# Optimization experiments

Hardware: AMD Instinct MI355X
Metric: run time of the kernel (lower is better)

The kernel has to match this reference:

```python
import jax, jax.numpy as jnp
import numpy as np

SCALE = 1.0  # module scale=1; dropout_p=0 so dropout is identity; selector is Identity


def setup_inputs() -> dict:
    key = jax.random.key(0)
    k0, k1, k2, k3, k4 = jax.random.split(key, 5)
    B, S, DIN, DOUT, P, R = 4, 2048, 4096, 4096, 5, 8
    x = jax.random.normal(k0, (B, S, DIN), dtype=jnp.float32)
    W = jax.random.normal(k1, (DOUT, DIN), dtype=jnp.float32) * 0.02   # nn.Linear weight [out, in]
    lora_down = jax.random.normal(k2, (P, DIN, R), dtype=jnp.float32) * 0.02
    lora_up = jax.random.normal(k3, (P, R, DOUT), dtype=jnp.float32) * 0.02
    lora_route = jax.random.normal(k4, (P, DIN, P), dtype=jnp.float32) * 0.02
    return {"x": x, "W": W, "lora_down": lora_down, "lora_up": lora_up,
            "lora_route": lora_route, "task_id": 4}


def reference(x, W, lora_down, lora_up, lora_route, task_id):
    tid = task_id  # Python int (static), tid > 1 branch
    # Routing: logits over the first (tid-1) experts using route table of task tid
    logits = jnp.einsum('bsi,ij->bsj', x, lora_route[tid - 1, :, :tid - 1])  # [B,S,tid-1]
    omegas = jax.nn.softmax(logits, axis=-1)
    # Previous experts: (lora_down[j] @ lora_up[j]).detach() -> stop_gradient.
    # Keep low-rank structure: z = x @ down  [B,S,J,R], then weight and project up.
    down_prev = jax.lax.stop_gradient(lora_down[:tid - 1])  # [J, DIN, R]
    up_prev = jax.lax.stop_gradient(lora_up[:tid - 1])      # [J, R, DOUT]
    z = jnp.einsum('bsi,jir->bsjr', x, down_prev)           # [B,S,J,R] small (R=8)
    delta_prev = jnp.einsum('bsjr,jro->bso', z * omegas[..., None], up_prev)
    # Current expert (j == tid-1): live params, no gating weight
    cur = (x @ lora_down[tid - 1]) @ lora_up[tid - 1]       # [B,S,DOUT]
    delta = SCALE * (delta_prev + cur)
    return x @ W.T + delta
```

## Files before the change

### kernel.cpp

```cpp
#include <hip/hip_runtime.h>
#include <hip/hip_bf16.h>

typedef unsigned short u16;
typedef __attribute__((ext_vector_type(8))) __bf16 bf16x8;
typedef __attribute__((ext_vector_type(4))) float f32x4;

#define DIN 4096
#define DOUT 4096
#define MROWS 8192

__device__ __forceinline__ u16 f2bf(float f) {
  unsigned int u = __float_as_uint(f);
  u += 0x7fffu + ((u >> 16) & 1u);
  return (u16)(u >> 16);
}

__device__ __forceinline__ void gl2lds16(const void* g, void* l) {
  __builtin_amdgcn_global_load_lds(
      (const __attribute__((address_space(1))) unsigned int*)g,
      (__attribute__((address_space(3))) unsigned int*)l, 16, 0, 0);
}

__global__ __launch_bounds__(256) void prep_all(
    const float* __restrict__ x, const float* __restrict__ W,
    const float* __restrict__ up, const float* __restrict__ route,
    const float* __restrict__ down,
    u16* __restrict__ Xb, u16* __restrict__ Wb,
    u16* __restrict__ Ub, u16* __restrict__ Wt) {
  const size_t NT = 2048 * 256;
  const size_t gtid = (size_t)blockIdx.x * 256 + threadIdx.x;

  if (gtid < 4096) {
    const int n = (int)gtid;
    union { u16 us[32]; uint4 q[4]; } o;
    #pragma unroll
    for (int c = 0; c < 32; ++c) o.us[c] = f2bf(up[(size_t)c * DOUT + n]);
    uint4* dst = (uint4*)(Ub + (size_t)n * 32);
    #pragma unroll
    for (int q = 0; q < 4; ++q) dst[q] = o.q[q];
  }

  if (gtid < 49152) {
    const int c = (int)(gtid >> 10);
    const int k0 = ((int)gtid & 1023) * 4;
    const float* route3 = route + 3 * DIN * 5;
    float v[4];
    #pragma unroll
    for (int j = 0; j < 4; ++j) {
      int k = k0 + j;
      float f;
      if (c < 3)       f = route3[(size_t)k * 5 + c];
      else if (c < 35) f = down[(size_t)((c - 3) >> 3) * DIN * 8 + (size_t)k * 8 + ((c - 3) & 7)];
      else             f = 0.f;
      v[j] = f;
    }
    ushort4 o;
    o.x = f2bf(v[0]); o.y = f2bf(v[1]); o.z = f2bf(v[2]); o.w = f2bf(v[3]);
    *(ushort4*)(Wt + (size_t)c * DIN + k0) = o;
  }

  #pragma unroll 4
  for (int it = 0; it < 16; ++it) {
    size_t i = gtid + (size_t)it * NT;
    float4 v = ((const float4*)x)[i];
    ushort4 o;
    o.x = f2bf(v.x); o.y = f2bf(v.y); o.z = f2bf(v.z); o.w = f2bf(v.w);
    ((ushort4*)Xb)[i] = o;
  }

  #pragma unroll 4
  for (int it = 0; it < 8; ++it) {
    size_t i = gtid + (size_t)it * NT;
    float4 v = ((const float4*)W)[i];
    ushort4 o;
    o.x = f2bf(v.x); o.y = f2bf(v.y); o.z = f2bf(v.z); o.w = f2bf(v.w);
    ((ushort4*)Wb)[i] = o;
  }
}

__global__ __launch_bounds__(256) void coeffgemm(
    const u16* __restrict__ Xb, const u16* __restrict__ Wt,
    float* __restrict__ Pw) {
  __shared__ __align__(16) u16 As[64 * 64];
  __shared__ __align__(16) u16 Bs[48 * 64];
  const int tid = threadIdx.x;
  const int m0 = blockIdx.x * 64;
  const int kb = blockIdx.y * 512;
  const int lane = tid & 63;
  const int w = tid >> 6;
  const int wr = w * 16;
  const int fm = lane & 15;
  const int xr = fm & 7;
  const int qd = lane >> 4;

  f32x4 acc[3];
  #pragma unroll
  for (int j = 0; j < 3; ++j) acc[j] = (f32x4){0.f, 0.f, 0.f, 0.f};

  const int arow = tid >> 3;
  const int ac = ((tid & 7) ^ (arow & 7)) * 8;
  const u16* gA = Xb + (size_t)(m0 + arow) * DIN + kb + ac;
  const u16* gBt = Wt + (size_t)arow * DIN + kb + ac;

  for (int kc = 0; kc < 512; kc += 64) {
    gl2lds16(gBt + kc, Bs + tid * 8);
    if (tid < 128)
      gl2lds16(gBt + 32 * DIN + kc, Bs + (256 + tid) * 8);
    gl2lds16(gA + kc, As + tid * 8);
    gl2lds16(gA + 32 * DIN + kc, As + (256 + tid) * 8);
    __syncthreads();
    #pragma unroll
    for (int kk = 0; kk < 64; kk += 32) {
      const int q = (kk >> 3) + qd;
      bf16x8 af = *(const bf16x8*)(As + (wr + fm) * 64 + ((q ^ xr) << 3));
      bf16x8 bfr[3];
      #pragma unroll
      for (int j = 0; j < 3; ++j)
        bfr[j] = *(const bf16x8*)(Bs + (j * 16 + fm) * 64 + ((q ^ xr) << 3));
      #pragma unroll
      for (int j = 0; j < 3; ++j)
        acc[j] = __builtin_amdgcn_mfma_f32_16x16x32_bf16(af, bfr[j], acc[j], 0, 0, 0);
    }
    __syncthreads();
  }
  const int em = (lane >> 4) * 4;
  const int en = lane & 15;
  const size_t pbase = (size_t)blockIdx.y * MROWS;
  #pragma unroll
  for (int j = 0; j < 3; ++j)
    #pragma unroll
    for (int r = 0; r < 4; ++r)
      Pw[(pbase + m0 + wr + em + r) * 48 + j * 16 + en] = acc[j][r];
}

__global__ __launch_bounds__(256) void reduce_coeff(const float* __restrict__ Pw,
                                                    u16* __restrict__ Cb) {
  const int tid = threadIdx.x;
  const int rl = tid >> 2;
  const int cg = tid & 3;
  const int m = blockIdx.x * 64 + rl;
  const int lane = tid & 63;

  float s[12];
  #pragma unroll
  for (int q = 0; q < 12; ++q) s[q] = 0.f;
  for (int sp = 0; sp < 8; ++sp) {
    const float4* p = (const float4*)(Pw + ((size_t)sp * MROWS + m) * 48 + cg * 12);
    #pragma unroll
    for (int q = 0; q < 3; ++q) {
      float4 v = p[q];
      s[q * 4 + 0] += v.x; s[q * 4 + 1] += v.y;
      s[q * 4 + 2] += v.z; s[q * 4 + 3] += v.w;
    }
  }
  const int src = lane & ~3;
  const float L0 = __shfl(s[0], src);
  const float L1 = __shfl(s[1], src);
  const float L2 = __shfl(s[2], src);
  const float mx = fmaxf(L0, fmaxf(L1, L2));
  const float e0 = __expf(L0 - mx), e1 = __expf(L1 - mx), e2 = __expf(L2 - mx);
  const float inv = 1.f / (e0 + e1 + e2);
  const float om0 = e0 * inv, om1 = e1 * inv, om2 = e2 * inv;
  #pragma unroll
  for (int j = 0; j < 12; ++j) {
    const int G = cg * 12 + j;
    if (G >= 3 && G < 35) {
      const float wgt = (G < 11) ? om0 : (G < 19) ? om1 : (G < 27) ? om2 : 1.f;
      Cb[(size_t)m * 32 + (G - 3)] = f2bf(s[j] * wgt);
    }
  }
}


#define MF(a, b, c) __builtin_amdgcn_mfma_f32_16x16x32_bf16(a, b, c, 0, 0, 0)

#define MROW(A, I) \
  acc[I][0] = MF(A, bfr0, acc[I][0]); \
  acc[I][1] = MF(A, bfr1, acc[I][1]); \
  acc[I][2] = MF(A, bfr2, acc[I][2]); \
  acc[I][3] = MF(A, bfr3, acc[I][3]);

#define VM4 asm volatile("s_waitcnt vmcnt(4)" ::: "memory")
#define VM0 asm volatile("s_waitcnt vmcnt(0)" ::: "memory")

#define STA(REG, KOFF) { const u16* s_ = gA + (KOFF); \
  gl2lds16(s_, dA + (REG) * 8192); \
  gl2lds16(s_ + 128 * 4096, dA + (REG) * 8192 + 4096); }
#define STB(REG, KOFF) { const u16* s_ = gB + (KOFF); \
  gl2lds16(s_, dB + (REG) * 8192); \
  gl2lds16(s_ + 128 * 4096, dB + (REG) * 8192 + 4096); }
#define STC { const u16* s_ = Cb + (size_t)(m0 + gr1) * 32 + kc1; \
  gl2lds16(s_, dA); gl2lds16(s_ + 128 * 32, dA + 4096); }
#define STU { const u16* s_ = Ub + (size_t)(n0 + gr1) * 32 + kc1; \
  gl2lds16(s_, dB); gl2lds16(s_ + 128 * 32, dB + 4096); }

#define PH(REG, IH, LOADB, ISSUE, VMX) { \
  const u16* ap_ = sm + (REG) * 8192 + wmoff + (IH) * 2048 + off0; \
  bf16x8 af0 = *(const bf16x8*)(ap_); \
  bf16x8 af1 = *(const bf16x8*)(ap_ + 512); \
  bf16x8 af2 = *(const bf16x8*)(ap_ + 1024); \
  bf16x8 af3 = *(const bf16x8*)(ap_ + 1536); \
  if (LOADB) { \
    const u16* bp_ = sm + 32768 + (REG) * 8192 + wnoff + off0; \
    bfr0 = *(const bf16x8*)(bp_); \
    bfr1 = *(const bf16x8*)(bp_ + 512); \
    bfr2 = *(const bf16x8*)(bp_ + 1024); \
    bfr3 = *(const bf16x8*)(bp_ + 1536); \
  } \
  ISSUE; \
  asm volatile("" ::: "memory"); \
  __builtin_amdgcn_s_barrier(); \
  __builtin_amdgcn_s_setprio(1); \
  MROW(af0, (IH) * 4 + 0) \
  MROW(af1, (IH) * 4 + 1) \
  MROW(af2, (IH) * 4 + 2) \
  MROW(af3, (IH) * 4 + 3) \
  __builtin_amdgcn_s_setprio(0); \
  VMX; \
  asm volatile("" ::: "memory"); \
  __builtin_amdgcn_s_barrier(); \
}

#define TILE(B, I1, I2, I3, I4, VMX) { \
  bf16x8 bfr0, bfr1, bfr2, bfr3; \
  PH((B) * 2 + 0, 0, 1, I1, (void)0) \
  PH((B) * 2 + 0, 1, 0, I2, (void)0) \
  PH((B) * 2 + 1, 0, 1, I3, (void)0) \
  PH((B) * 2 + 1, 1, 0, I4, VMX) \
}

__global__ __launch_bounds__(512, 2) void gemm_fused8(
    const u16* __restrict__ Xb, const u16* __restrict__ Wb,
    const u16* __restrict__ Cb, const u16* __restrict__ Ub,
    float* __restrict__ out) {
  __shared__ __align__(16) u16 sm[65536];
  const int tid = threadIdx.x;
  const int bid = blockIdx.x;
  const int wg = (bid & 7) * 64 + (bid >> 3);
  const int mt = wg >> 4;
  const int nt = wg & 15;
  const int m0 = mt * 256;
  const int n0 = nt * 256;
  const int lane = tid & 63;
  const int w = tid >> 6;
  const int wm = w >> 2;
  const int wn = w & 3;
  const int fm = lane & 15;
  const int qd = lane >> 4;
  const int off0 = (fm >> 1) * 64 + (((((fm & 1) << 2) | qd)) ^ (fm >> 1)) * 8;
  const int wmoff = wm * 4096;
  const int wnoff = wn * 2048;

  const int c1 = (tid & 7) ^ ((tid >> 3) & 7);
  const int gr1 = 2 * (tid >> 3) + (c1 >> 2);
  const int kc1 = (c1 & 3) * 8;
  const u16* gA = Xb + (size_t)(m0 + gr1) * 4096 + kc1;
  const u16* gB = Wb + (size_t)(n0 + gr1) * 4096 + kc1;
  u16* dA = sm + tid * 8;
  u16* dB = sm + 32768 + tid * 8;

  f32x4 acc[8][4];
  #pragma unroll
  for (int i = 0; i < 8; ++i)
    #pragma unroll
    for (int j = 0; j < 4; ++j) acc[i][j] = (f32x4){0.f, 0.f, 0.f, 0.f};

  STA(0, 0)  STB(0, 0)
  STA(1, 32) STB(1, 32)
  STA(2, 64) STB(2, 64)
  VM4;
  asm volatile("" ::: "memory");
  __builtin_amdgcn_s_barrier();

  for (int T = 0; T < 62; T += 2) {
    TILE(0, STA(3, T * 64 + 96),  STB(3, T * 64 + 96),
            STA(0, T * 64 + 128), STB(0, T * 64 + 128), VM4)
    TILE(1, STA(1, T * 64 + 160), STB(1, T * 64 + 160),
            STA(2, T * 64 + 192), STB(2, T * 64 + 192), VM4)
  }
  TILE(0, STA(3, 4064), STB(3, 4064), (void)0, (void)0, VM0)
  TILE(1, STC, STU, (void)0, (void)0, VM0)

  {
    const u16* ap = sm + wmoff + off0;
    const u16* bp = sm + 32768 + wnoff + off0;
    bf16x8 bfr0 = *(const bf16x8*)(bp);
    bf16x8 bfr1 = *(const bf16x8*)(bp + 512);
    bf16x8 bfr2 = *(const bf16x8*)(bp + 1024);
    bf16x8 bfr3 = *(const bf16x8*)(bp + 1536);
    #pragma unroll
    for (int i = 0; i < 8; ++i) {
      bf16x8 a = *(const bf16x8*)(ap + i * 512);
      acc[i][0] = MF(a, bfr0, acc[i][0]);
      acc[i][1] = MF(a, bfr1, acc[i][1]);
      acc[i][2] = MF(a, bfr2, acc[i][2]);
      acc[i][3] = MF(a, bfr3, acc[i][3]);
    }
  }

  const int em = qd * 4;
  const int en = fm;
  const size_t obase = (size_t)(m0 + wm * 128) * DOUT + n0 + wn * 64 + en;
  #pragma unroll
  for (int i = 0; i < 8; ++i)
    #pragma unroll
    for (int j = 0; j < 4; ++j)
      #pragma unroll
      for (int r = 0; r < 4; ++r)
        out[obase + (size_t)(i * 16 + em + r) * DOUT + j * 16] = acc[i][j][r];
}

extern "C" void kernel_launch(void* const* d_in, const int* in_sizes, int n_in,
                              void* d_out, int out_size, void* d_ws, size_t ws_size,
                              hipStream_t stream) {
  const float* x     = (const float*)d_in[0];
  const float* W     = (const float*)d_in[1];
  const float* down  = (const float*)d_in[2];
  const float* up    = (const float*)d_in[3];
  const float* route = (const float*)d_in[4];
  float* out = (float*)d_out;

  char* ws = (char*)d_ws;
  u16*   Xb = (u16*)ws;
  u16*   Wb = (u16*)(ws + 67108864);
  u16*   Cb = (u16*)(ws + 100663296);
  u16*   Ub = (u16*)(ws + 101187584);
  u16*   Wt = (u16*)(ws + 101449728);
  float* Pw = (float*)(ws + 101842944);

  prep_all<<<2048, 256, 0, stream>>>(x, W, up, route, down, Xb, Wb, Ub, Wt);
  coeffgemm<<<dim3(128, 8), 256, 0, stream>>>(Xb, Wt, Pw);
  reduce_coeff<<<128, 256, 0, stream>>>(Pw, Cb);
  gemm_fused8<<<512, 512, 0, stream>>>(Xb, Wb, Cb, Ub, out);
}
```

Baseline: 533.0 us.

## Fuse coefficient GEMM split-K reduction and softmax into one kernel

Replaces the split-K coefficient GEMM (128x8 blocks writing partials to global memory) and the separate reduce/softmax kernel with one kernel. Each block handles 32 rows over the full K, with the four waves each taking a K-slice, then reduces across waves in LDS and applies the softmax gating before writing bf16 coefficients. This removes a kernel launch and the global round-trip of the partial sums. The cost is fewer blocks (256 instead of 1024), each doing a longer serial K loop, which may lower occupancy and latency hiding.

```diff
diff --git a/kernel.cpp b/kernel.cpp
--- a/kernel.cpp
+++ b/kernel.cpp
@@ -78,96 +78,114 @@
   }
 }
 
-__global__ __launch_bounds__(256) void coeffgemm(
+__global__ __launch_bounds__(256) void coeff_full(
     const u16* __restrict__ Xb, const u16* __restrict__ Wt,
-    float* __restrict__ Pw) {
-  __shared__ __align__(16) u16 As[64 * 64];
-  __shared__ __align__(16) u16 Bs[48 * 64];
+    u16* __restrict__ Cb) {
+  __shared__ __align__(16) u16 lds[20480];
+  u16* As = lds;
+  u16* Bs = lds + 8192;
   const int tid = threadIdx.x;
-  const int m0 = blockIdx.x * 64;
-  const int kb = blockIdx.y * 512;
+  const int m0 = blockIdx.x * 32;
   const int lane = tid & 63;
   const int w = tid >> 6;
-  const int wr = w * 16;
   const int fm = lane & 15;
   const int xr = fm & 7;
   const int qd = lane >> 4;
 
-  f32x4 acc[3];
+  f32x4 acc[2][3];
   #pragma unroll
-  for (int j = 0; j < 3; ++j) acc[j] = (f32x4){0.f, 0.f, 0.f, 0.f};
+  for (int i = 0; i < 2; ++i)
+    #pragma unroll
+    for (int j = 0; j < 3; ++j) acc[i][j] = (f32x4){0.f, 0.f, 0.f, 0.f};
 
   const int arow = tid >> 3;
   const int ac = ((tid & 7) ^ (arow & 7)) * 8;
-  const u16* gA = Xb + (size_t)(m0 + arow) * DIN + kb + ac;
-  const u16* gBt = Wt + (size_t)arow * DIN + kb + ac;
-
-  for (int kc = 0; kc < 512; kc += 64) {
-    gl2lds16(gBt + kc, Bs + tid * 8);
-    if (tid < 128)
-      gl2lds16(gBt + 32 * DIN + kc, Bs + (256 + tid) * 8);
-    gl2lds16(gA + kc, As + tid * 8);
-    gl2lds16(gA + 32 * DIN + kc, As + (256 + tid) * 8);
+  const u16* gA = Xb + (size_t)(m0 + arow) * DIN + ac;
+  const u16* gBt = Wt + (size_t)arow * DIN + ac;
+
+  for (int s = 0; s < 16; ++s) {
+    const int kb = s * 256;
+    #pragma unroll
+    for (int u = 0; u < 4; ++u) {
+      gl2lds16(gA + kb + u * 64, As + u * 2048 + tid * 8);
+      gl2lds16(gBt + kb + u * 64, Bs + u * 3072 + tid * 8);
+      if (tid < 128)
+        gl2lds16(gBt + 32 * DIN + kb + u * 64, Bs + u * 3072 + (256 + tid) * 8);
+    }
     __syncthreads();
+    const u16* Aw = As + w * 2048;
+    const u16* Bw = Bs + w * 3072;
     #pragma unroll
     for (int kk = 0; kk < 64; kk += 32) {
       const int q = (kk >> 3) + qd;
-      bf16x8 af = *(const bf16x8*)(As + (wr + fm) * 64 + ((q ^ xr) << 3));
-      bf16x8 bfr[3];
+      const int co = (q ^ xr) << 3;
+      bf16x8 af[2], bfr[3];
+      #pragma unroll
+      for (int mi = 0; mi < 2; ++mi)
+        af[mi] = *(const bf16x8*)(Aw + (mi * 16 + fm) * 64 + co);
       #pragma unroll
       for (int j = 0; j < 3; ++j)
-        bfr[j] = *(const bf16x8*)(Bs + (j * 16 + fm) * 64 + ((q ^ xr) << 3));
-      #pragma unroll
-      for (int j = 0; j < 3; ++j)
-        acc[j] = __builtin_amdgcn_mfma_f32_16x16x32_bf16(af, bfr[j], acc[j], 0, 0, 0);
+        bfr[j] = *(const bf16x8*)(Bw + (j * 16 + fm) * 64 + co);
+      #pragma unroll
+      for (int mi = 0; mi < 2; ++mi)
+        #pragma unroll
+        for (int j = 0; j < 3; ++j)
+          acc[mi][j] = __builtin_amdgcn_mfma_f32_16x16x32_bf16(af[mi], bfr[j], acc[mi][j], 0, 0, 0);
     }
     __syncthreads();
   }
-  const int em = (lane >> 4) * 4;
-  const int en = lane & 15;
-  const size_t pbase = (size_t)blockIdx.y * MROWS;
+
+  float* Pf = (float*)lds;
+  const int em = qd * 4;
+  const int en = fm;
   #pragma unroll
-  for (int j = 0; j < 3; ++j)
-    #pragma unroll
-    for (int r = 0; r < 4; ++r)
-      Pw[(pbase + m0 + wr + em + r) * 48 + j * 16 + en] = acc[j][r];
-}
-
-__global__ __launch_bounds__(256) void reduce_coeff(const float* __restrict__ Pw,
-                                                    u16* __restrict__ Cb) {
-  const int tid = threadIdx.x;
-  const int rl = tid >> 2;
-  const int cg = tid & 3;
-  const int m = blockIdx.x * 64 + rl;
-  const int lane = tid & 63;
-
-  float s[12];
-  #pragma unroll
-  for (int q = 0; q < 12; ++q) s[q] = 0.f;
-  for (int sp = 0; sp < 8; ++sp) {
-    const float4* p = (const float4*)(Pw + ((size_t)sp * MROWS + m) * 48 + cg * 12);
-    #pragma unroll
-    for (int q = 0; q < 3; ++q) {
-      float4 v = p[q];
-      s[q * 4 + 0] += v.x; s[q * 4 + 1] += v.y;
-      s[q * 4 + 2] += v.z; s[q * 4 + 3] += v.w;
-    }
-  }
-  const int src = lane & ~3;
-  const float L0 = __shfl(s[0], src);
-  const float L1 = __shfl(s[1], src);
-  const float L2 = __shfl(s[2], src);
-  const float mx = fmaxf(L0, fmaxf(L1, L2));
-  const float e0 = __expf(L0 - mx), e1 = __expf(L1 - mx), e2 = __expf(L2 - mx);
-  const float inv = 1.f / (e0 + e1 + e2);
-  const float om0 = e0 * inv, om1 = e1 * inv, om2 = e2 * inv;
-  #pragma unroll
-  for (int j = 0; j < 12; ++j) {
-    const int G = cg * 12 + j;
-    if (G >= 3 && G < 35) {
-      const float wgt = (G < 11) ? om0 : (G < 19) ? om1 : (G < 27) ? om2 : 1.f;
-      Cb[(size_t)m * 32 + (G - 3)] = f2bf(s[j] * wgt);
-    }
+  for (int mi = 0; mi < 2; ++mi)
+    #pragma unroll
+    for (int j = 0; j < 3; ++j)
+      #pragma unroll
+      for (int r = 0; r < 4; ++r)
+        Pf[(size_t)(w * 32 + mi * 16 + em + r) * 48 + j * 16 + en] = acc[mi][j][r];
+  __syncthreads();
+
+  float* Sf = (float*)(lds + 12288);
+  {
+    const int row = tid >> 3;
+    const int cb = (tid & 7) * 6;
+    #pragma unroll
+    for (int c = 0; c < 6; ++c) {
+      const int col = cb + c;
+      float v = Pf[(size_t)(0 * 32 + row) * 48 + col]
+              + Pf[(size_t)(1 * 32 + row) * 48 + col]
+              + Pf[(size_t)(2 * 32 + row) * 48 + col]
+              + Pf[(size_t)(3 * 32 + row) * 48 + col];
+      Sf[row * 48 + col] = v;
+    }
+  }
+  __syncthreads();
+
+  float* om = (float*)(lds + 15360);
+  if (tid < 32) {
+    const float L0 = Sf[tid * 48 + 0], L1 = Sf[tid * 48 + 1], L2 = Sf[tid * 48 + 2];
+    const float mx = fmaxf(L0, fmaxf(L1, L2));
+    const float e0 = __expf(L0 - mx), e1 = __expf(L1 - mx), e2 = __expf(L2 - mx);
+    const float inv = 1.f / (e0 + e1 + e2);
+    om[tid * 3 + 0] = e0 * inv; om[tid * 3 + 1] = e1 * inv; om[tid * 3 + 2] = e2 * inv;
+  }
+  __syncthreads();
+
+  {
+    const int row = tid >> 3;
+    const int c4 = (tid & 7) * 4;
+    u16 tmp[4];
+    #pragma unroll
+    for (int c = 0; c < 4; ++c) {
+      const int oc = c4 + c;
+      const int ex = oc >> 3;
+      const float wgt = (ex < 3) ? om[row * 3 + ex] : 1.f;
+      tmp[c] = f2bf(Sf[row * 48 + 3 + oc] * wgt);
+    }
+    ushort4 o; o.x = tmp[0]; o.y = tmp[1]; o.z = tmp[2]; o.w = tmp[3];
+    *(ushort4*)(Cb + (size_t)(m0 + row) * 32 + c4) = o;
   }
 }
 
@@ -326,10 +344,8 @@
   u16*   Cb = (u16*)(ws + 100663296);
   u16*   Ub = (u16*)(ws + 101187584);
   u16*   Wt = (u16*)(ws + 101449728);
-  float* Pw = (float*)(ws + 101842944);
 
   prep_all<<<2048, 256, 0, stream>>>(x, W, up, route, down, Xb, Wb, Ub, Wt);
-  coeffgemm<<<dim3(128, 8), 256, 0, stream>>>(Xb, Wt, Pw);
-  reduce_coeff<<<128, 256, 0, stream>>>(Pw, Cb);
+  coeff_full<<<256, 256, 0, stream>>>(Xb, Wt, Cb);
   gemm_fused8<<<512, 512, 0, stream>>>(Xb, Wb, Cb, Ub, out);
 }
```

After: 553.9 us. 1.04x slower.
